# Performance work log

Measured on AMD Instinct MI355X. Metric: run time of the kernel, lower is better.

## Reference

```python
import jax, jax.numpy as jnp
import numpy as np

S = 7          # side
B = 2          # boxes per cell
C = 20         # classes
L = S * S      # grid cells
NOOBJ = 0.5 * 1.0
OBJ   = 0.5 * 1.0
CLS   = 0.5 * 1.0
COORD = 0.5 * 5.0


def setup_inputs() -> dict:
    key = jax.random.key(0)
    k1, k2, k3 = jax.random.split(key, 3)
    n = 16384
    preds = jax.random.uniform(k1, (n, L * (C + 5 * B)), dtype=jnp.float32)
    labels = jax.random.uniform(k2, (n, L * (1 + C + 4)), dtype=jnp.float32)
    lab = labels.reshape(n, L, 1 + C + 4)
    obj_flag = (jax.random.uniform(k3, (n, L)) < 0.15).astype(jnp.float32)
    lab = lab.at[:, :, 0].set(obj_flag)
    labels = lab.reshape(n, -1)
    return {"preds": preds, "labels": labels}


def _iou(t, o):
    # t, o: [..., 4] boxes in (cx, cy, w, h); returns [...]
    left   = jnp.maximum(t[..., 0] - 0.5 * t[..., 2], o[..., 0] - 0.5 * o[..., 2])
    right  = jnp.minimum(t[..., 0] + 0.5 * t[..., 2], o[..., 0] + 0.5 * o[..., 2])
    top    = jnp.maximum(t[..., 1] - 0.5 * t[..., 3], o[..., 1] - 0.5 * o[..., 3])
    bottom = jnp.minimum(t[..., 1] + 0.5 * t[..., 3], o[..., 1] + 0.5 * o[..., 3])
    w = right - left
    h = bottom - top
    invalid = (w < 0) | (h < 0)
    inter = jnp.where(invalid, 0.0, w * h)
    union = t[..., 2] * t[..., 3] + o[..., 2] * o[..., 3] - inter
    return jnp.where(invalid, 0.0, inter / jnp.maximum(union, 1e-12))


def reference(preds, labels):
    n = preds.shape[0]
    pcls  = preds[:, : L * C].reshape(n, L, C)                       # [n,L,C]
    pconf = preds[:, L * C : L * C + L * B].reshape(n, L, B)          # [n,L,B]
    pbox  = preds[:, L * C + L * B :].reshape(n, L, B, 4)             # [n,L,B,4]

    lab  = labels.reshape(n, L, 1 + C + 4)
    obj  = lab[:, :, 0] != 0                                          # [n,L]
    tcls = lab[:, :, 1 : 1 + C]                                       # [n,L,C]
    tbox = lab[:, :, 1 + C :]                                         # [n,L,4] raw

    # --- best-box selection (on detached predictions, like .detach() in torch) ---
    o_raw = jax.lax.stop_gradient(pbox)
    o = jnp.concatenate([o_raw[..., :2] / S, o_raw[..., 2:] ** 2], axis=-1)      # [n,L,B,4]
    t = jnp.concatenate([tbox[..., :2] / S, tbox[..., 2:]], axis=-1)[:, :, None] # [n,L,1,4]
    t = jax.lax.stop_gradient(t)

    iou  = _iou(t, o)                                                 # [n,L,B]
    rmse = jnp.sqrt(jnp.sum((t - o) ** 2, axis=-1))                   # [n,L,B]
    max_iou = jnp.max(iou, axis=-1)
    # if any IoU>0 pick first argmax of IoU, else first argmin of RMSE (best_rmse init 20)
    best = jnp.where(max_iou > 0, jnp.argmax(iou, axis=-1), jnp.argmin(rmse, axis=-1))  # [n,L]
    best_iou = jnp.take_along_axis(iou, best[:, :, None], axis=-1)[..., 0]        # [n,L]

    onehot = jnp.arange(B) == best[:, :, None]                        # [n,L,B]
    mask_best = obj[:, :, None] & onehot

    # confidence delta: noobject everywhere, overwritten at best box of object cells
    conf_delta = jnp.where(mask_best,
                           OBJ * (best_iou[:, :, None] - pconf) ** 2,
                           NOOBJ * pconf ** 2)

    # class delta (object cells only)
    cls_delta = jnp.where(obj[:, :, None], CLS * (tcls - pcls) ** 2, 0.0)

    # coord delta at best box: raw truth x,y and sqrt(truth w,h) vs raw preds
    pbest = jnp.take_along_axis(pbox, best[:, :, None, None], axis=2)[:, :, 0]    # [n,L,4]
    ttarget = jnp.concatenate([tbox[..., :2], jnp.sqrt(tbox[..., 2:])], axis=-1)  # [n,L,4]
    coord_delta = jnp.where(obj[:, :, None], COORD * (ttarget - pbest) ** 2, 0.0)

    return jnp.nansum(conf_delta) + jnp.nansum(cls_delta) + jnp.nansum(coord_delta)
```

## Files before the change

### kernel.cpp

```cpp
#include <hip/hip_runtime.h>


#define L_CELLS 49
#define PRED_ROW 1470
#define LAB_ROW 1225
#define CONF_BASE 980
#define BOX_BASE 1078
#define W_NOOBJ 0.5f
#define W_OBJ 0.5f
#define W_CLS 0.5f
#define W_COORD 2.5f
#define INV_S (1.0f / 7.0f)

__global__ __launch_bounds__(256) void yolo_loss_kernel(
    const float* __restrict__ preds, const float* __restrict__ labels,
    float* __restrict__ ws) {
  __shared__ float4 labs4[4][312];

  const int tid = threadIdx.x;
  const int w = tid >> 6;
  const int lane = tid & 63;
  const int s = blockIdx.x * 4 + w;

  size_t g0 = (size_t)s * LAB_ROW;
  size_t a = g0 & ~(size_t)3;
  int off = (int)(g0 - a);
  for (int i = lane; i < 307; i += 64) {
    labs4[w][i] = *(const float4*)(labels + a + 4 * (size_t)i);
  }

  const float* lab = (const float*)labs4[w] + off;
  const float* rp = preds + (size_t)s * PRED_ROW;

  float acc = 0.0f;
  if (lane < L_CELLS) {
    const int l = lane;
    float2 cf = *(const float2*)(rp + CONF_BASE + 2 * l);
    float c0 = cf.x, c1 = cf.y;
    float objf = lab[25 * l];

    if (objf != 0.0f) {
      float bx[8];
#pragma unroll
      for (int k = 0; k < 4; ++k) {
        float2 v = *(const float2*)(rp + BOX_BASE + 8 * l + 2 * k);
        bx[2 * k] = v.x;
        bx[2 * k + 1] = v.y;
      }
      float tx = lab[25 * l + 21], ty = lab[25 * l + 22];
      float tw = lab[25 * l + 23], th = lab[25 * l + 24];
      float t0 = tx * INV_S, t1 = ty * INV_S, t2 = tw, t3 = th;

      float iou[2], rmse2[2];
#pragma unroll
      for (int b = 0; b < 2; ++b) {
        float o0 = bx[4 * b + 0] * INV_S;
        float o1 = bx[4 * b + 1] * INV_S;
        float o2 = bx[4 * b + 2] * bx[4 * b + 2];
        float o3 = bx[4 * b + 3] * bx[4 * b + 3];
        float left = fmaxf(t0 - 0.5f * t2, o0 - 0.5f * o2);
        float right = fminf(t0 + 0.5f * t2, o0 + 0.5f * o2);
        float top = fmaxf(t1 - 0.5f * t3, o1 - 0.5f * o3);
        float bot = fminf(t1 + 0.5f * t3, o1 + 0.5f * o3);
        float wd = right - left;
        float h = bot - top;
        bool invalid = (wd < 0.0f) || (h < 0.0f);
        float inter = invalid ? 0.0f : wd * h;
        float uni = t2 * t3 + o2 * o3 - inter;
        iou[b] = invalid ? 0.0f : inter / fmaxf(uni, 1e-12f);
        float d0 = t0 - o0, d1 = t1 - o1, d2 = t2 - o2, d3 = t3 - o3;
        rmse2[b] = d0 * d0 + d1 * d1 + d2 * d2 + d3 * d3;
      }

      float max_iou = fmaxf(iou[0], iou[1]);
      int best;
      if (max_iou > 0.0f)
        best = (iou[1] > iou[0]) ? 1 : 0;
      else
        best = (rmse2[1] < rmse2[0]) ? 1 : 0;
      float best_iou = iou[best];

      float cb = (best == 0) ? c0 : c1;
      float co = (best == 0) ? c1 : c0;
      float db = best_iou - cb;
      acc += W_OBJ * db * db + W_NOOBJ * co * co;

      float clsacc = 0.0f;
#pragma unroll
      for (int k = 0; k < 10; ++k) {
        float2 p = *(const float2*)(rp + 20 * l + 2 * k);
        float d0 = lab[25 * l + 1 + 2 * k] - p.x;
        float d1 = lab[25 * l + 2 + 2 * k] - p.y;
        clsacc += d0 * d0 + d1 * d1;
      }
      acc += W_CLS * clsacc;

      float e0 = tx - bx[best * 4 + 0];
      float e1 = ty - bx[best * 4 + 1];
      float e2 = sqrtf(tw) - bx[best * 4 + 2];
      float e3 = sqrtf(th) - bx[best * 4 + 3];
      acc += W_COORD * (e0 * e0 + e1 * e1 + e2 * e2 + e3 * e3);
    } else {
      acc += W_NOOBJ * (c0 * c0 + c1 * c1);
    }
  }

#pragma unroll
  for (int o = 32; o > 0; o >>= 1) acc += __shfl_down(acc, o);

  __shared__ float wsum[4];
  if (lane == 0) wsum[w] = acc;
  __syncthreads();
  if (tid == 0) ws[blockIdx.x] = wsum[0] + wsum[1] + wsum[2] + wsum[3];
}

__global__ __launch_bounds__(256) void final_reduce_kernel(
    const float* __restrict__ ws, float* __restrict__ out, int m) {
  float acc = 0.0f;
  for (int i = threadIdx.x; i < m; i += 256) acc += ws[i];
#pragma unroll
  for (int o = 32; o > 0; o >>= 1) acc += __shfl_down(acc, o);
  __shared__ float wsum[4];
  int wave = threadIdx.x >> 6;
  int lane = threadIdx.x & 63;
  if (lane == 0) wsum[wave] = acc;
  __syncthreads();
  if (threadIdx.x == 0) out[0] = wsum[0] + wsum[1] + wsum[2] + wsum[3];
}

extern "C" void kernel_launch(void* const* d_in, const int* in_sizes, int n_in,
                              void* d_out, int out_size, void* d_ws, size_t ws_size,
                              hipStream_t stream) {
  const float* preds = (const float*)d_in[0];
  const float* labels = (const float*)d_in[1];
  float* out = (float*)d_out;
  float* ws = (float*)d_ws;
  int n = in_sizes[0] / PRED_ROW;
  int blocks = n / 4;

  yolo_loss_kernel<<<blocks, 256, 0, stream>>>(preds, labels, ws);
  final_reduce_kernel<<<1, 256, 0, stream>>>(ws, out, blocks);
}
```

Before: 189.1 us.

## Map threads to flat grid cells with four cells each, dropping LDS label staging

Instead of one wave per sample with 15 of 64 lanes idle and a shared-memory copy of the whole label row, each thread now handles four grid cells taken from a flat cell index spaced a quarter of the total apart. It issues the objectness, confidence and box-target loads for all four cells up front to expose memory-level parallelism. Class labels are read straight from global memory and only for object cells. The final reduce becomes a single 1024-thread pass with no loop. The trade-offs are strided, uncoalesced label loads, fewer blocks, and an implicit assumption that the cell count divides evenly by 1024.

```diff
diff --git a/kernel.cpp b/kernel.cpp
--- a/kernel.cpp
+++ b/kernel.cpp
@@ -14,41 +14,48 @@
 
 __global__ __launch_bounds__(256) void yolo_loss_kernel(
     const float* __restrict__ preds, const float* __restrict__ labels,
-    float* __restrict__ ws) {
-  __shared__ float4 labs4[4][312];
+    float* __restrict__ ws, int quarter) {
+  const int t = blockIdx.x * 256 + threadIdx.x;
 
-  const int tid = threadIdx.x;
-  const int w = tid >> 6;
-  const int lane = tid & 63;
-  const int s = blockIdx.x * 4 + w;
-
-  size_t g0 = (size_t)s * LAB_ROW;
-  size_t a = g0 & ~(size_t)3;
-  int off = (int)(g0 - a);
-  for (int i = lane; i < 307; i += 64) {
-    labs4[w][i] = *(const float4*)(labels + a + 4 * (size_t)i);
+  const float* labc[4];
+  const float* rp[4];
+  int l[4];
+  float objf[4];
+  float2 cf[4];
+  float tb[4][4];
+#pragma unroll
+  for (int j = 0; j < 4; ++j) {
+    int c = t + j * quarter;
+    int s = c / L_CELLS;
+    int li = c - s * L_CELLS;
+    const float* lb = labels + (size_t)s * LAB_ROW + 25 * li;
+    const float* pp = preds + (size_t)s * PRED_ROW;
+    labc[j] = lb;
+    rp[j] = pp;
+    l[j] = li;
+    objf[j] = lb[0];
+    cf[j] = *(const float2*)(pp + CONF_BASE + 2 * li);
+    tb[j][0] = lb[21];
+    tb[j][1] = lb[22];
+    tb[j][2] = lb[23];
+    tb[j][3] = lb[24];
   }
 
-  const float* lab = (const float*)labs4[w] + off;
-  const float* rp = preds + (size_t)s * PRED_ROW;
-
   float acc = 0.0f;
-  if (lane < L_CELLS) {
-    const int l = lane;
-    float2 cf = *(const float2*)(rp + CONF_BASE + 2 * l);
-    float c0 = cf.x, c1 = cf.y;
-    float objf = lab[25 * l];
-
-    if (objf != 0.0f) {
+#pragma unroll
+  for (int j = 0; j < 4; ++j) {
+    float c0 = cf[j].x, c1 = cf[j].y;
+    if (objf[j] != 0.0f) {
+      const float* pp = rp[j];
+      const int li = l[j];
       float bx[8];
 #pragma unroll
       for (int k = 0; k < 4; ++k) {
-        float2 v = *(const float2*)(rp + BOX_BASE + 8 * l + 2 * k);
+        float2 v = *(const float2*)(pp + BOX_BASE + 8 * li + 2 * k);
         bx[2 * k] = v.x;
         bx[2 * k + 1] = v.y;
       }
-      float tx = lab[25 * l + 21], ty = lab[25 * l + 22];
-      float tw = lab[25 * l + 23], th = lab[25 * l + 24];
+      float tx = tb[j][0], ty = tb[j][1], tw = tb[j][2], th = tb[j][3];
       float t0 = tx * INV_S, t1 = ty * INV_S, t2 = tw, t3 = th;
 
       float iou[2], rmse2[2];
@@ -85,12 +92,13 @@
       float db = best_iou - cb;
       acc += W_OBJ * db * db + W_NOOBJ * co * co;
 
+      const float* lb = labc[j];
       float clsacc = 0.0f;
 #pragma unroll
       for (int k = 0; k < 10; ++k) {
-        float2 p = *(const float2*)(rp + 20 * l + 2 * k);
-        float d0 = lab[25 * l + 1 + 2 * k] - p.x;
-        float d1 = lab[25 * l + 2 + 2 * k] - p.y;
+        float2 p = *(const float2*)(pp + 20 * li + 2 * k);
+        float d0 = lb[1 + 2 * k] - p.x;
+        float d1 = lb[2 + 2 * k] - p.y;
         clsacc += d0 * d0 + d1 * d1;
       }
       acc += W_CLS * clsacc;
@@ -109,23 +117,29 @@
   for (int o = 32; o > 0; o >>= 1) acc += __shfl_down(acc, o);
 
   __shared__ float wsum[4];
-  if (lane == 0) wsum[w] = acc;
-  __syncthreads();
-  if (tid == 0) ws[blockIdx.x] = wsum[0] + wsum[1] + wsum[2] + wsum[3];
-}
-
-__global__ __launch_bounds__(256) void final_reduce_kernel(
-    const float* __restrict__ ws, float* __restrict__ out, int m) {
-  float acc = 0.0f;
-  for (int i = threadIdx.x; i < m; i += 256) acc += ws[i];
-#pragma unroll
-  for (int o = 32; o > 0; o >>= 1) acc += __shfl_down(acc, o);
-  __shared__ float wsum[4];
   int wave = threadIdx.x >> 6;
   int lane = threadIdx.x & 63;
   if (lane == 0) wsum[wave] = acc;
   __syncthreads();
-  if (threadIdx.x == 0) out[0] = wsum[0] + wsum[1] + wsum[2] + wsum[3];
+  if (threadIdx.x == 0) ws[blockIdx.x] = wsum[0] + wsum[1] + wsum[2] + wsum[3];
+}
+
+__global__ __launch_bounds__(1024) void final_reduce_kernel(
+    const float* __restrict__ ws, float* __restrict__ out, int m) {
+  float acc = (threadIdx.x < m) ? ws[threadIdx.x] : 0.0f;
+#pragma unroll
+  for (int o = 32; o > 0; o >>= 1) acc += __shfl_down(acc, o);
+  __shared__ float wsum[16];
+  int wave = threadIdx.x >> 6;
+  int lane = threadIdx.x & 63;
+  if (lane == 0) wsum[wave] = acc;
+  __syncthreads();
+  if (threadIdx.x == 0) {
+    float s = 0.0f;
+#pragma unroll
+    for (int i = 0; i < 16; ++i) s += wsum[i];
+    out[0] = s;
+  }
 }
 
 extern "C" void kernel_launch(void* const* d_in, const int* in_sizes, int n_in,
@@ -136,8 +150,10 @@
   float* out = (float*)d_out;
   float* ws = (float*)d_ws;
   int n = in_sizes[0] / PRED_ROW;
-  int blocks = n / 4;
+  int total = n * L_CELLS;
+  int quarter = total / 4;
+  int blocks = quarter / 256;
 
-  yolo_loss_kernel<<<blocks, 256, 0, stream>>>(preds, labels, ws);
-  final_reduce_kernel<<<1, 256, 0, stream>>>(ws, out, blocks);
+  yolo_loss_kernel<<<blocks, 256, 0, stream>>>(preds, labels, ws, quarter);
+  final_reduce_kernel<<<1, 1024, 0, stream>>>(ws, out, blocks);
 }
```

Measured after the change: 193.3 us. 2.3% more time.
